# Kernel tuning notes

Measured on AMD Instinct MI355X. Metric: run time of the kernel, lower is better.

## Reference

```python
import jax, jax.numpy as jnp
import numpy as np
import math

CHUNK_SIZE = 1024

def setup_inputs() -> dict:
    key = jax.random.key(0)
    kq, kk, kv = jax.random.split(key, 3)
    B, H, T, D = 2, 16, 4096, 128
    return {
        "query": jax.random.normal(kq, (B, H, T, D), dtype=jnp.float32),
        "key": jax.random.normal(kk, (B, H, T, D), dtype=jnp.float32),
        "value": jax.random.normal(kv, (B, H, T, D), dtype=jnp.float32),
    }

def _chunked_causal_attention(query, key, value, chunk_size=CHUNK_SIZE):
    B, H, T, D = query.shape
    scale = 1.0 / math.sqrt(D)
    num_chunks = (T + chunk_size - 1) // chunk_size
    outputs = []
    for ci in range(num_chunks):
        start = ci * chunk_size
        end = min((ci + 1) * chunk_size, T)
        q_chunk = query[:, :, start:end, :]            # [B,H,c,D]
        k_chunk = key[:, :, :end, :]                   # [B,H,end,D]
        v_chunk = value[:, :, :end, :]                 # [B,H,end,D]
        scores = jnp.einsum('bhqd,bhkd->bhqk', q_chunk, k_chunk) * scale
        # causal mask: key position must be <= query position
        q_idx = jnp.arange(start, end)[:, None]        # [c,1]
        k_idx = jnp.arange(end)[None, :]               # [1,end]
        scores = jnp.where(k_idx <= q_idx, scores, -jnp.inf)
        weights = jax.nn.softmax(scores, axis=-1)
        outputs.append(jnp.einsum('bhqk,bhkd->bhqd', weights, v_chunk))
    return jnp.concatenate(outputs, axis=2)

def reference(query, key, value):
    return _chunked_causal_attention(query, key, value)
```

## Files before the change

### kernel.cpp

```cpp
#include <hip/hip_runtime.h>
#include <stdint.h>


typedef __bf16 bf16x8 __attribute__((ext_vector_type(8)));
typedef float f32x16 __attribute__((ext_vector_type(16)));
typedef unsigned short u16x8 __attribute__((ext_vector_type(8)));
typedef unsigned int u32x2 __attribute__((ext_vector_type(2)));

#define T_SEQ 4096
#define D_HEAD 128
#define BQ 128
#define NQT (T_SEQ / BQ)
#define BK 64
#define KSTR 136
#define VSTR 72

__device__ __forceinline__ unsigned int pack_bf2(float a, float b) {
    unsigned int ua = __builtin_bit_cast(unsigned int, a) + 0x8000u;
    unsigned int ub = __builtin_bit_cast(unsigned int, b) + 0x8000u;
    return __builtin_amdgcn_perm(ub, ua, 0x07060302);
}

__global__ __launch_bounds__(256, 2) void fa_fwd(
    const float* __restrict__ Qg, const float* __restrict__ Kg,
    const float* __restrict__ Vg, float* __restrict__ Og)
{
    __shared__ unsigned short K_lds[BK * KSTR];
    __shared__ unsigned short Vt_lds[D_HEAD * VSTR];

    const int tid  = threadIdx.x;
    const int w    = tid >> 6;
    const int lane = tid & 63;
    const int r    = lane & 31;
    const int h    = lane >> 5;

    const int bid = (int)blockIdx.x;
    const int g   = bid & 255;
    const int j   = bid >> 8;
    const int t   = g & 7;
    const int bh  = g >> 3;
    const int qt  = (j == 0) ? (31 - t) : (j == 1) ? t : (j == 2) ? (16 + t) : (15 - t);
    const int q0  = qt * BQ;

    const float* Qb = Qg + (size_t)bh * T_SEQ * D_HEAD;
    const float* Kb = Kg + (size_t)bh * T_SEQ * D_HEAD;
    const float* Vb = Vg + (size_t)bh * T_SEQ * D_HEAD;
    float*       Ob = Og + (size_t)bh * T_SEQ * D_HEAD;

    const int qw      = q0 + 32 * w;
    const int q_lane  = qw + r;
    const int qw_last = qw + 31;

    const float qscale = 0.08838834764831845f * 1.4426950408889634f;
    bf16x8 qf[8];
#pragma unroll
    for (int c = 0; c < 8; ++c) {
        const float* src = Qb + (size_t)q_lane * D_HEAD + c * 16 + h * 8;
        float4 f0 = *(const float4*)(src);
        float4 f1 = *(const float4*)(src + 4);
        unsigned int u0 = pack_bf2(f0.x * qscale, f0.y * qscale);
        unsigned int u1 = pack_bf2(f0.z * qscale, f0.w * qscale);
        unsigned int u2 = pack_bf2(f1.x * qscale, f1.y * qscale);
        unsigned int u3 = pack_bf2(f1.z * qscale, f1.w * qscale);
        u16x8 u = { (unsigned short)u0, (unsigned short)(u0 >> 16),
                    (unsigned short)u1, (unsigned short)(u1 >> 16),
                    (unsigned short)u2, (unsigned short)(u2 >> 16),
                    (unsigned short)u3, (unsigned short)(u3 >> 16) };
        qf[c] = __builtin_bit_cast(bf16x8, u);
    }

    f32x16 o[4];
#pragma unroll
    for (int mt = 0; mt < 4; ++mt) o[mt] = (f32x16)0.0f;
    float m_run = -1e30f, l_run = 0.0f;

    const int krow = tid >> 5;
    const int kd0  = (tid & 31) * 4;
    const int vd   = tid & 127;
    const int vhh  = tid >> 7;

    float4 kpre[8];
    float  vpre[8][4];

#pragma unroll
    for (int p = 0; p < 8; ++p)
        kpre[p] = *(const float4*)(Kb + (size_t)(p * 8 + krow) * D_HEAD + kd0);
#pragma unroll
    for (int p = 0; p < 8; ++p) {
        const int kv0 = p * 8 + vhh * 4;
        const float* vs = Vb + (size_t)kv0 * D_HEAD + vd;
        vpre[p][0] = vs[0];
        vpre[p][1] = vs[D_HEAD];
        vpre[p][2] = vs[2 * D_HEAD];
        vpre[p][3] = vs[3 * D_HEAD];
    }

    const int ntiles = 2 * qt + 2;
    for (int kt = 0; kt < ntiles; ++kt) {
        const int kbase = kt * BK;
        __syncthreads();

#pragma unroll
        for (int p = 0; p < 8; ++p) {
            u32x2 u;
            u[0] = pack_bf2(kpre[p].x, kpre[p].y);
            u[1] = pack_bf2(kpre[p].z, kpre[p].w);
            *(u32x2*)&K_lds[(p * 8 + krow) * KSTR + kd0] = u;
        }
#pragma unroll
        for (int p = 0; p < 8; ++p) {
            u32x2 u;
            u[0] = pack_bf2(vpre[p][0], vpre[p][1]);
            u[1] = pack_bf2(vpre[p][2], vpre[p][3]);
            const int col = (p >> 1) * 16 + vhh * 8 + (p & 1) * 4;
            *(u32x2*)&Vt_lds[vd * VSTR + col] = u;
        }
        __syncthreads();

        if (kt + 1 < ntiles) {
            const int nb = kbase + BK;
#pragma unroll
            for (int p = 0; p < 8; ++p)
                kpre[p] = *(const float4*)(Kb + (size_t)(nb + p * 8 + krow) * D_HEAD + kd0);
#pragma unroll
            for (int p = 0; p < 8; ++p) {
                const int kv0 = nb + p * 8 + vhh * 4;
                const float* vs = Vb + (size_t)kv0 * D_HEAD + vd;
                vpre[p][0] = vs[0];
                vpre[p][1] = vs[D_HEAD];
                vpre[p][2] = vs[2 * D_HEAD];
                vpre[p][3] = vs[3 * D_HEAD];
            }
        }

        if (kbase > qw_last) continue;

        f32x16 s[2];
        s[0] = (f32x16)0.0f; s[1] = (f32x16)0.0f;
        __builtin_amdgcn_s_setprio(1);
#pragma unroll
        for (int t2 = 0; t2 < 2; ++t2) {
#pragma unroll
            for (int c = 0; c < 8; ++c) {
                u16x8 raw = *(const u16x8*)&K_lds[(t2 * 32 + r) * KSTR + c * 16 + h * 8];
                bf16x8 a = __builtin_bit_cast(bf16x8, raw);
                s[t2] = __builtin_amdgcn_mfma_f32_32x32x16_bf16(a, qf[c], s[t2], 0, 0, 0);
            }
        }
        __builtin_amdgcn_s_setprio(0);

        if (kbase + BK - 1 > qw) {
#pragma unroll
            for (int t2 = 0; t2 < 2; ++t2)
#pragma unroll
                for (int g2 = 0; g2 < 16; ++g2) {
                    int kv = kbase + t2 * 32 + (g2 & 3) + 8 * (g2 >> 2) + 4 * h;
                    if (kv > q_lane) s[t2][g2] = -1e30f;
                }
        }

        float mloc = -1e30f;
#pragma unroll
        for (int t2 = 0; t2 < 2; ++t2)
#pragma unroll
            for (int g2 = 0; g2 < 16; ++g2) mloc = fmaxf(mloc, s[t2][g2]);
        mloc = fmaxf(mloc, __shfl_xor(mloc, 32, 64));

        if (!__all(mloc - m_run <= 8.0f)) {
            const float m_new = fmaxf(m_run, mloc);
            const float alpha = __builtin_amdgcn_exp2f(m_run - m_new);
            l_run *= alpha;
#pragma unroll
            for (int mt = 0; mt < 4; ++mt)
#pragma unroll
                for (int g2 = 0; g2 < 16; ++g2) o[mt][g2] *= alpha;
            m_run = m_new;
        }

        float rsum = 0.0f;
#pragma unroll
        for (int t2 = 0; t2 < 2; ++t2)
#pragma unroll
            for (int g2 = 0; g2 < 16; ++g2) {
                float p = __builtin_amdgcn_exp2f(s[t2][g2] - m_run);
                s[t2][g2] = p;
                rsum += p;
            }
        rsum += __shfl_xor(rsum, 32, 64);
        l_run += rsum;

        bf16x8 pf[4];
#pragma unroll
        for (int c = 0; c < 4; ++c) {
            const int tt = c >> 1;
            const int g0 = (c & 1) * 8;
            unsigned int u0 = pack_bf2(s[tt][g0 + 0], s[tt][g0 + 1]);
            unsigned int u1 = pack_bf2(s[tt][g0 + 2], s[tt][g0 + 3]);
            unsigned int u2 = pack_bf2(s[tt][g0 + 4], s[tt][g0 + 5]);
            unsigned int u3 = pack_bf2(s[tt][g0 + 6], s[tt][g0 + 7]);
            u16x8 u = { (unsigned short)u0, (unsigned short)(u0 >> 16),
                        (unsigned short)u1, (unsigned short)(u1 >> 16),
                        (unsigned short)u2, (unsigned short)(u2 >> 16),
                        (unsigned short)u3, (unsigned short)(u3 >> 16) };
            pf[c] = __builtin_bit_cast(bf16x8, u);
        }

        __builtin_amdgcn_s_setprio(1);
#pragma unroll
        for (int mt = 0; mt < 4; ++mt) {
#pragma unroll
            for (int c = 0; c < 4; ++c) {
                u16x8 raw = *(const u16x8*)&Vt_lds[(mt * 32 + r) * VSTR + c * 16 + h * 8];
                bf16x8 a = __builtin_bit_cast(bf16x8, raw);
                o[mt] = __builtin_amdgcn_mfma_f32_32x32x16_bf16(a, pf[c], o[mt], 0, 0, 0);
            }
        }
        __builtin_amdgcn_s_setprio(0);
    }

    const float inv = 1.0f / l_run;
#pragma unroll
    for (int mt = 0; mt < 4; ++mt)
#pragma unroll
        for (int g4 = 0; g4 < 4; ++g4) {
            float4 vv;
            vv.x = o[mt][g4 * 4 + 0] * inv;
            vv.y = o[mt][g4 * 4 + 1] * inv;
            vv.z = o[mt][g4 * 4 + 2] * inv;
            vv.w = o[mt][g4 * 4 + 3] * inv;
            const int dd = mt * 32 + g4 * 8 + h * 4;
            *(float4*)(Ob + (size_t)q_lane * D_HEAD + dd) = vv;
        }
}

extern "C" void kernel_launch(void* const* d_in, const int* in_sizes, int n_in,
                              void* d_out, int out_size, void* d_ws, size_t ws_size,
                              hipStream_t stream) {
    const float* Q = (const float*)d_in[0];
    const float* K = (const float*)d_in[1];
    const float* V = (const float*)d_in[2];
    float* O = (float*)d_out;
    dim3 grid(NQT * 32, 1, 1);
    fa_fwd<<<grid, 256, 0, stream>>>(Q, K, V, O);
}
```

Baseline: 473.0 us.

## Pair complementary query tiles per block and split KV tiles across two thread groups

Each 512-thread block now handles a long and a short causal query tile (pr and 31-pr), which gives every block the same amount of work. Within the block, two 256-thread groups take alternating 64-key tiles, each with its own K/V LDS buffers. Their partial softmax states (m, l and the O accumulator) are merged through LDS reused as scratch, in two halves to stay within capacity. This adds parallelism per query tile and removes tail imbalance. The cost is extra merge traffic and barriers, and the 512-thread, 2-block launch bound may force register spills.

Measured after the change: 513.7 us. 8.6% more time.

```diff
diff --git a/kernel.cpp b/kernel.cpp
--- a/kernel.cpp
+++ b/kernel.cpp
@@ -21,110 +21,81 @@
     return __builtin_amdgcn_perm(ub, ua, 0x07060302);
 }
 
-__global__ __launch_bounds__(256, 2) void fa_fwd(
+__global__ __launch_bounds__(512, 2) void fa_fwd(
     const float* __restrict__ Qg, const float* __restrict__ Kg,
     const float* __restrict__ Vg, float* __restrict__ Og)
 {
-    __shared__ unsigned short K_lds[BK * KSTR];
-    __shared__ unsigned short Vt_lds[D_HEAD * VSTR];
-
-    const int tid  = threadIdx.x;
-    const int w    = tid >> 6;
+    __shared__ unsigned short K_lds[2][BK * KSTR];
+    __shared__ unsigned short Vt_lds[2][D_HEAD * VSTR];
+
+    const int tid  = (int)threadIdx.x;
+    const int grp  = tid >> 8;
+    const int gtid = tid & 255;
+    const int w    = gtid >> 6;
     const int lane = tid & 63;
     const int r    = lane & 31;
     const int h    = lane >> 5;
 
     const int bid = (int)blockIdx.x;
-    const int g   = bid & 255;
-    const int j   = bid >> 8;
-    const int t   = g & 7;
-    const int bh  = g >> 3;
-    const int qt  = (j == 0) ? (31 - t) : (j == 1) ? t : (j == 2) ? (16 + t) : (15 - t);
-    const int q0  = qt * BQ;
+    const int pr  = bid & 15;
+    const int bh  = bid >> 4;
 
     const float* Qb = Qg + (size_t)bh * T_SEQ * D_HEAD;
     const float* Kb = Kg + (size_t)bh * T_SEQ * D_HEAD;
     const float* Vb = Vg + (size_t)bh * T_SEQ * D_HEAD;
     float*       Ob = Og + (size_t)bh * T_SEQ * D_HEAD;
 
-    const int qw      = q0 + 32 * w;
-    const int q_lane  = qw + r;
-    const int qw_last = qw + 31;
+    unsigned short* Kl = &K_lds[grp][0];
+    unsigned short* Vl = &Vt_lds[grp][0];
+    float* cb  = (float*)&K_lds[0][0];
+    float* cml = (float*)&Vt_lds[0][0];
+
+    const int krow = gtid >> 5;
+    const int kd0  = (gtid & 31) * 4;
+    const int vd   = gtid & 127;
+    const int vhh  = gtid >> 7;
 
     const float qscale = 0.08838834764831845f * 1.4426950408889634f;
-    bf16x8 qf[8];
-#pragma unroll
-    for (int c = 0; c < 8; ++c) {
-        const float* src = Qb + (size_t)q_lane * D_HEAD + c * 16 + h * 8;
-        float4 f0 = *(const float4*)(src);
-        float4 f1 = *(const float4*)(src + 4);
-        unsigned int u0 = pack_bf2(f0.x * qscale, f0.y * qscale);
-        unsigned int u1 = pack_bf2(f0.z * qscale, f0.w * qscale);
-        unsigned int u2 = pack_bf2(f1.x * qscale, f1.y * qscale);
-        unsigned int u3 = pack_bf2(f1.z * qscale, f1.w * qscale);
-        u16x8 u = { (unsigned short)u0, (unsigned short)(u0 >> 16),
-                    (unsigned short)u1, (unsigned short)(u1 >> 16),
-                    (unsigned short)u2, (unsigned short)(u2 >> 16),
-                    (unsigned short)u3, (unsigned short)(u3 >> 16) };
-        qf[c] = __builtin_bit_cast(bf16x8, u);
-    }
-
-    f32x16 o[4];
-#pragma unroll
-    for (int mt = 0; mt < 4; ++mt) o[mt] = (f32x16)0.0f;
-    float m_run = -1e30f, l_run = 0.0f;
-
-    const int krow = tid >> 5;
-    const int kd0  = (tid & 31) * 4;
-    const int vd   = tid & 127;
-    const int vhh  = tid >> 7;
-
-    float4 kpre[8];
-    float  vpre[8][4];
-
-#pragma unroll
-    for (int p = 0; p < 8; ++p)
-        kpre[p] = *(const float4*)(Kb + (size_t)(p * 8 + krow) * D_HEAD + kd0);
-#pragma unroll
-    for (int p = 0; p < 8; ++p) {
-        const int kv0 = p * 8 + vhh * 4;
-        const float* vs = Vb + (size_t)kv0 * D_HEAD + vd;
-        vpre[p][0] = vs[0];
-        vpre[p][1] = vs[D_HEAD];
-        vpre[p][2] = vs[2 * D_HEAD];
-        vpre[p][3] = vs[3 * D_HEAD];
-    }
-
-    const int ntiles = 2 * qt + 2;
-    for (int kt = 0; kt < ntiles; ++kt) {
-        const int kbase = kt * BK;
-        __syncthreads();
-
-#pragma unroll
-        for (int p = 0; p < 8; ++p) {
-            u32x2 u;
-            u[0] = pack_bf2(kpre[p].x, kpre[p].y);
-            u[1] = pack_bf2(kpre[p].z, kpre[p].w);
-            *(u32x2*)&K_lds[(p * 8 + krow) * KSTR + kd0] = u;
-        }
-#pragma unroll
-        for (int p = 0; p < 8; ++p) {
-            u32x2 u;
-            u[0] = pack_bf2(vpre[p][0], vpre[p][1]);
-            u[1] = pack_bf2(vpre[p][2], vpre[p][3]);
-            const int col = (p >> 1) * 16 + vhh * 8 + (p & 1) * 4;
-            *(u32x2*)&Vt_lds[vd * VSTR + col] = u;
-        }
-        __syncthreads();
-
-        if (kt + 1 < ntiles) {
-            const int nb = kbase + BK;
+
+    for (int phase = 0; phase < 2; ++phase) {
+        const int qt = (phase == 0) ? (NQT - 1 - pr) : pr;
+        const int q0 = qt * BQ;
+        const int qw      = q0 + 32 * w;
+        const int q_lane  = qw + r;
+        const int qw_last = qw + 31;
+
+        bf16x8 qf[8];
+#pragma unroll
+        for (int c = 0; c < 8; ++c) {
+            const float* src = Qb + (size_t)q_lane * D_HEAD + c * 16 + h * 8;
+            float4 f0 = *(const float4*)(src);
+            float4 f1 = *(const float4*)(src + 4);
+            unsigned int u0 = pack_bf2(f0.x * qscale, f0.y * qscale);
+            unsigned int u1 = pack_bf2(f0.z * qscale, f0.w * qscale);
+            unsigned int u2 = pack_bf2(f1.x * qscale, f1.y * qscale);
+            unsigned int u3 = pack_bf2(f1.z * qscale, f1.w * qscale);
+            u16x8 u = { (unsigned short)u0, (unsigned short)(u0 >> 16),
+                        (unsigned short)u1, (unsigned short)(u1 >> 16),
+                        (unsigned short)u2, (unsigned short)(u2 >> 16),
+                        (unsigned short)u3, (unsigned short)(u3 >> 16) };
+            qf[c] = __builtin_bit_cast(bf16x8, u);
+        }
+
+        f32x16 o[4];
+#pragma unroll
+        for (int mt = 0; mt < 4; ++mt) o[mt] = (f32x16)0.0f;
+        float m_run = -1e30f, l_run = 0.0f;
+
+        float4 kpre[8];
+        float  vpre[8][4];
+        {
+            const int tb = grp * BK;
 #pragma unroll
             for (int p = 0; p < 8; ++p)
-                kpre[p] = *(const float4*)(Kb + (size_t)(nb + p * 8 + krow) * D_HEAD + kd0);
+                kpre[p] = *(const float4*)(Kb + (size_t)(tb + p * 8 + krow) * D_HEAD + kd0);
 #pragma unroll
             for (int p = 0; p < 8; ++p) {
-                const int kv0 = nb + p * 8 + vhh * 4;
+                const int kv0 = tb + p * 8 + vhh * 4;
                 const float* vs = Vb + (size_t)kv0 * D_HEAD + vd;
                 vpre[p][0] = vs[0];
                 vpre[p][1] = vs[D_HEAD];
@@ -133,104 +104,187 @@
             }
         }
 
-        if (kbase > qw_last) continue;
-
-        f32x16 s[2];
-        s[0] = (f32x16)0.0f; s[1] = (f32x16)0.0f;
-        __builtin_amdgcn_s_setprio(1);
-#pragma unroll
-        for (int t2 = 0; t2 < 2; ++t2) {
-#pragma unroll
-            for (int c = 0; c < 8; ++c) {
-                u16x8 raw = *(const u16x8*)&K_lds[(t2 * 32 + r) * KSTR + c * 16 + h * 8];
-                bf16x8 a = __builtin_bit_cast(bf16x8, raw);
-                s[t2] = __builtin_amdgcn_mfma_f32_32x32x16_bf16(a, qf[c], s[t2], 0, 0, 0);
-            }
-        }
-        __builtin_amdgcn_s_setprio(0);
-
-        if (kbase + BK - 1 > qw) {
+        const int niter = qt + 1;
+        for (int i = 0; i < niter; ++i) {
+            const int kbase = (2 * i + grp) * BK;
+            __syncthreads();
+
+#pragma unroll
+            for (int p = 0; p < 8; ++p) {
+                u32x2 u;
+                u[0] = pack_bf2(kpre[p].x, kpre[p].y);
+                u[1] = pack_bf2(kpre[p].z, kpre[p].w);
+                *(u32x2*)&Kl[(p * 8 + krow) * KSTR + kd0] = u;
+            }
+#pragma unroll
+            for (int p = 0; p < 8; ++p) {
+                u32x2 u;
+                u[0] = pack_bf2(vpre[p][0], vpre[p][1]);
+                u[1] = pack_bf2(vpre[p][2], vpre[p][3]);
+                const int col = (p >> 1) * 16 + vhh * 8 + (p & 1) * 4;
+                *(u32x2*)&Vl[vd * VSTR + col] = u;
+            }
+            __syncthreads();
+
+            if (i + 1 < niter) {
+                const int nb = (2 * (i + 1) + grp) * BK;
+#pragma unroll
+                for (int p = 0; p < 8; ++p)
+                    kpre[p] = *(const float4*)(Kb + (size_t)(nb + p * 8 + krow) * D_HEAD + kd0);
+#pragma unroll
+                for (int p = 0; p < 8; ++p) {
+                    const int kv0 = nb + p * 8 + vhh * 4;
+                    const float* vs = Vb + (size_t)kv0 * D_HEAD + vd;
+                    vpre[p][0] = vs[0];
+                    vpre[p][1] = vs[D_HEAD];
+                    vpre[p][2] = vs[2 * D_HEAD];
+                    vpre[p][3] = vs[3 * D_HEAD];
+                }
+            }
+
+            if (kbase > qw_last) continue;
+
+            f32x16 s[2];
+            s[0] = (f32x16)0.0f; s[1] = (f32x16)0.0f;
+            __builtin_amdgcn_s_setprio(1);
+#pragma unroll
+            for (int t2 = 0; t2 < 2; ++t2) {
+#pragma unroll
+                for (int c = 0; c < 8; ++c) {
+                    u16x8 raw = *(const u16x8*)&Kl[(t2 * 32 + r) * KSTR + c * 16 + h * 8];
+                    bf16x8 a = __builtin_bit_cast(bf16x8, raw);
+                    s[t2] = __builtin_amdgcn_mfma_f32_32x32x16_bf16(a, qf[c], s[t2], 0, 0, 0);
+                }
+            }
+            __builtin_amdgcn_s_setprio(0);
+
+            if (kbase + BK - 1 > qw) {
+#pragma unroll
+                for (int t2 = 0; t2 < 2; ++t2)
+#pragma unroll
+                    for (int g2 = 0; g2 < 16; ++g2) {
+                        int kv = kbase + t2 * 32 + (g2 & 3) + 8 * (g2 >> 2) + 4 * h;
+                        if (kv > q_lane) s[t2][g2] = -1e30f;
+                    }
+            }
+
+            float mloc = -1e30f;
 #pragma unroll
             for (int t2 = 0; t2 < 2; ++t2)
 #pragma unroll
+                for (int g2 = 0; g2 < 16; ++g2) mloc = fmaxf(mloc, s[t2][g2]);
+            mloc = fmaxf(mloc, __shfl_xor(mloc, 32, 64));
+
+            if (!__all(mloc - m_run <= 8.0f)) {
+                const float m_new = fmaxf(m_run, mloc);
+                const float alpha = __builtin_amdgcn_exp2f(m_run - m_new);
+                l_run *= alpha;
+#pragma unroll
+                for (int mt = 0; mt < 4; ++mt)
+#pragma unroll
+                    for (int g2 = 0; g2 < 16; ++g2) o[mt][g2] *= alpha;
+                m_run = m_new;
+            }
+
+            float rsum = 0.0f;
+#pragma unroll
+            for (int t2 = 0; t2 < 2; ++t2)
+#pragma unroll
                 for (int g2 = 0; g2 < 16; ++g2) {
-                    int kv = kbase + t2 * 32 + (g2 & 3) + 8 * (g2 >> 2) + 4 * h;
-                    if (kv > q_lane) s[t2][g2] = -1e30f;
-                }
-        }
-
-        float mloc = -1e30f;
-#pragma unroll
-        for (int t2 = 0; t2 < 2; ++t2)
-#pragma unroll
-            for (int g2 = 0; g2 < 16; ++g2) mloc = fmaxf(mloc, s[t2][g2]);
-        mloc = fmaxf(mloc, __shfl_xor(mloc, 32, 64));
-
-        if (!__all(mloc - m_run <= 8.0f)) {
-            const float m_new = fmaxf(m_run, mloc);
-            const float alpha = __builtin_amdgcn_exp2f(m_run - m_new);
-            l_run *= alpha;
-#pragma unroll
-            for (int mt = 0; mt < 4; ++mt)
-#pragma unroll
-                for (int g2 = 0; g2 < 16; ++g2) o[mt][g2] *= alpha;
-            m_run = m_new;
-        }
-
-        float rsum = 0.0f;
-#pragma unroll
-        for (int t2 = 0; t2 < 2; ++t2)
-#pragma unroll
-            for (int g2 = 0; g2 < 16; ++g2) {
-                float p = __builtin_amdgcn_exp2f(s[t2][g2] - m_run);
-                s[t2][g2] = p;
-                rsum += p;
-            }
-        rsum += __shfl_xor(rsum, 32, 64);
-        l_run += rsum;
-
-        bf16x8 pf[4];
-#pragma unroll
-        for (int c = 0; c < 4; ++c) {
-            const int tt = c >> 1;
-            const int g0 = (c & 1) * 8;
-            unsigned int u0 = pack_bf2(s[tt][g0 + 0], s[tt][g0 + 1]);
-            unsigned int u1 = pack_bf2(s[tt][g0 + 2], s[tt][g0 + 3]);
-            unsigned int u2 = pack_bf2(s[tt][g0 + 4], s[tt][g0 + 5]);
-            unsigned int u3 = pack_bf2(s[tt][g0 + 6], s[tt][g0 + 7]);
-            u16x8 u = { (unsigned short)u0, (unsigned short)(u0 >> 16),
-                        (unsigned short)u1, (unsigned short)(u1 >> 16),
-                        (unsigned short)u2, (unsigned short)(u2 >> 16),
-                        (unsigned short)u3, (unsigned short)(u3 >> 16) };
-            pf[c] = __builtin_bit_cast(bf16x8, u);
-        }
-
-        __builtin_amdgcn_s_setprio(1);
-#pragma unroll
-        for (int mt = 0; mt < 4; ++mt) {
+                    float p = __builtin_amdgcn_exp2f(s[t2][g2] - m_run);
+                    s[t2][g2] = p;
+                    rsum += p;
+                }
+            rsum += __shfl_xor(rsum, 32, 64);
+            l_run += rsum;
+
+            bf16x8 pf[4];
 #pragma unroll
             for (int c = 0; c < 4; ++c) {
-                u16x8 raw = *(const u16x8*)&Vt_lds[(mt * 32 + r) * VSTR + c * 16 + h * 8];
-                bf16x8 a = __builtin_bit_cast(bf16x8, raw);
-                o[mt] = __builtin_amdgcn_mfma_f32_32x32x16_bf16(a, pf[c], o[mt], 0, 0, 0);
-            }
-        }
-        __builtin_amdgcn_s_setprio(0);
+                const int tt = c >> 1;
+                const int g0 = (c & 1) * 8;
+                unsigned int u0 = pack_bf2(s[tt][g0 + 0], s[tt][g0 + 1]);
+                unsigned int u1 = pack_bf2(s[tt][g0 + 2], s[tt][g0 + 3]);
+                unsigned int u2 = pack_bf2(s[tt][g0 + 4], s[tt][g0 + 5]);
+                unsigned int u3 = pack_bf2(s[tt][g0 + 6], s[tt][g0 + 7]);
+                u16x8 u = { (unsigned short)u0, (unsigned short)(u0 >> 16),
+                            (unsigned short)u1, (unsigned short)(u1 >> 16),
+                            (unsigned short)u2, (unsigned short)(u2 >> 16),
+                            (unsigned short)u3, (unsigned short)(u3 >> 16) };
+                pf[c] = __builtin_bit_cast(bf16x8, u);
+            }
+
+            __builtin_amdgcn_s_setprio(1);
+#pragma unroll
+            for (int mt = 0; mt < 4; ++mt) {
+#pragma unroll
+                for (int c = 0; c < 4; ++c) {
+                    u16x8 raw = *(const u16x8*)&Vl[(mt * 32 + r) * VSTR + c * 16 + h * 8];
+                    bf16x8 a = __builtin_bit_cast(bf16x8, raw);
+                    o[mt] = __builtin_amdgcn_mfma_f32_32x32x16_bf16(a, pf[c], o[mt], 0, 0, 0);
+                }
+            }
+            __builtin_amdgcn_s_setprio(0);
+        }
+
+        __syncthreads();
+        if (grp == 1) {
+            cml[gtid * 2 + 0] = m_run;
+            cml[gtid * 2 + 1] = l_run;
+#pragma unroll
+            for (int mt = 0; mt < 2; ++mt)
+#pragma unroll
+                for (int g2 = 0; g2 < 16; ++g2)
+                    cb[gtid * 33 + mt * 16 + g2] = o[mt][g2];
+        }
+        __syncthreads();
+        float aA = 1.0f, aB = 0.0f, linv = 0.0f;
+        if (grp == 0) {
+            const float mB = cml[gtid * 2 + 0];
+            const float lB = cml[gtid * 2 + 1];
+            const float m  = fmaxf(m_run, mB);
+            aA = __builtin_amdgcn_exp2f(m_run - m);
+            aB = __builtin_amdgcn_exp2f(mB - m);
+            linv = 1.0f / (l_run * aA + lB * aB);
+#pragma unroll
+            for (int mt = 0; mt < 2; ++mt)
+#pragma unroll
+                for (int g4 = 0; g4 < 4; ++g4) {
+                    const int b = gtid * 33 + mt * 16 + g4 * 4;
+                    float4 vv;
+                    vv.x = (o[mt][g4 * 4 + 0] * aA + cb[b + 0] * aB) * linv;
+                    vv.y = (o[mt][g4 * 4 + 1] * aA + cb[b + 1] * aB) * linv;
+                    vv.z = (o[mt][g4 * 4 + 2] * aA + cb[b + 2] * aB) * linv;
+                    vv.w = (o[mt][g4 * 4 + 3] * aA + cb[b + 3] * aB) * linv;
+                    const int dd = mt * 32 + g4 * 8 + h * 4;
+                    *(float4*)(Ob + (size_t)q_lane * D_HEAD + dd) = vv;
+                }
+        }
+        __syncthreads();
+        if (grp == 1) {
+#pragma unroll
+            for (int mt = 2; mt < 4; ++mt)
+#pragma unroll
+                for (int g2 = 0; g2 < 16; ++g2)
+                    cb[gtid * 33 + (mt - 2) * 16 + g2] = o[mt][g2];
+        }
+        __syncthreads();
+        if (grp == 0) {
+#pragma unroll
+            for (int mt = 2; mt < 4; ++mt)
+#pragma unroll
+                for (int g4 = 0; g4 < 4; ++g4) {
+                    const int b = gtid * 33 + (mt - 2) * 16 + g4 * 4;
+                    float4 vv;
+                    vv.x = (o[mt][g4 * 4 + 0] * aA + cb[b + 0] * aB) * linv;
+                    vv.y = (o[mt][g4 * 4 + 1] * aA + cb[b + 1] * aB) * linv;
+                    vv.z = (o[mt][g4 * 4 + 2] * aA + cb[b + 2] * aB) * linv;
+                    vv.w = (o[mt][g4 * 4 + 3] * aA + cb[b + 3] * aB) * linv;
+                    const int dd = mt * 32 + g4 * 8 + h * 4;
+                    *(float4*)(Ob + (size_t)q_lane * D_HEAD + dd) = vv;
+                }
+        }
     }
-
-    const float inv = 1.0f / l_run;
-#pragma unroll
-    for (int mt = 0; mt < 4; ++mt)
-#pragma unroll
-        for (int g4 = 0; g4 < 4; ++g4) {
-            float4 vv;
-            vv.x = o[mt][g4 * 4 + 0] * inv;
-            vv.y = o[mt][g4 * 4 + 1] * inv;
-            vv.z = o[mt][g4 * 4 + 2] * inv;
-            vv.w = o[mt][g4 * 4 + 3] * inv;
-            const int dd = mt * 32 + g4 * 8 + h * 4;
-            *(float4*)(Ob + (size_t)q_lane * D_HEAD + dd) = vv;
-        }
 }
 
 extern "C" void kernel_launch(void* const* d_in, const int* in_sizes, int n_in,
@@ -240,6 +294,6 @@
     const float* K = (const float*)d_in[1];
     const float* V = (const float*)d_in[2];
     float* O = (float*)d_out;
-    dim3 grid(NQT * 32, 1, 1);
-    fa_fwd<<<grid, 256, 0, stream>>>(Q, K, V, O);
+    dim3 grid((NQT / 2) * 32, 1, 1);
+    fa_fwd<<<grid, 512, 0, stream>>>(Q, K, V, O);
 }
```
